# Kernel tuning notes

Measured on AMD Instinct MI355X. Metric: run time of the kernel, lower is better.

## Reference

```python
import jax, jax.numpy as jnp
import numpy as np

H, W = 2048, 2048
S = 10            # depth_segments
BOTTOM_PCT = 1    # bottom_percent
P_MIX = 0.5       # p
F_SCALE = 2.0     # f


def setup_inputs() -> dict:
    key = jax.random.key(0)
    k1, k2 = jax.random.split(key)
    image = jax.random.uniform(k1, (3, H, W), dtype=jnp.float32)
    # the |d_nbr - d_ctr| < 1 threshold gives a non-trivial bilateral mask.
    depth = jax.random.uniform(k2, (H, W), dtype=jnp.float32) * 5.0
    mu0 = jnp.ones((), dtype=jnp.float32)
    mu1 = jnp.ones((), dtype=jnp.float32)
    mu2 = jnp.ones((), dtype=jnp.float32)
    return {"image": image, "depth": depth, "mu0": mu0, "mu1": mu1, "mu2": mu2}


def _eigm_forward(image, depth, mu0, mu1, mu2):
    Hh, Ww = depth.shape
    HW = Hh * Ww
    dt = image.dtype

    # --- ULAP depth prior: d = mu0 + mu1*max(g,b) + mu2*r ---
    r, g, b = image[0], image[1], image[2]
    d = mu0 + mu1 * jnp.maximum(g, b) + mu2 * r                    # [H,W]

    # --- per-depth-bin background light B_c and direct signal D_c ---
    bins = jnp.linspace(depth.min(), depth.max(), S + 1)           # [S+1]
    seg = (depth[None] >= bins[:-1, None, None]) & (depth[None] < bins[1:, None, None])  # [S,H,W] bool
    seg_flat = seg.reshape(S, HW)
    n = seg_flat.sum(axis=1)                                       # [S] pixels per bin

    min_rgb = image.min(axis=0).reshape(HW)                        # darkest channel per pixel
    vals = jnp.where(seg_flat, min_rgb[None, :], jnp.asarray(np.inf, dt))
    svals = jnp.sort(vals, axis=1)                                 # segment pixels first, inf padding last
    k = (n * BOTTOM_PCT) // 100                                    # topk(largest=False) count per bin
    take = jnp.arange(HW)[None, :] < k[:, None]
    B_c = jnp.sum(jnp.where(take, svals, jnp.asarray(0.0, dt)), axis=1) / k.astype(dt)  # [S]

    segf = seg.astype(dt)
    seg_mean = jnp.einsum('chw,shw->sc', image, segf) / n.astype(dt)[:, None]  # [S,3]
    D_seg = seg_mean - B_c[:, None]                                # [S,3] per-segment direct signal
    # scatter each segment's D_c to its pixels -> per-pixel map [1,3,H,W]
    D = jnp.einsum('shw,sc->chw', segf, D_seg)[None]

    # --- depth-thresholded 3x3 local average (bilateral-style stencil) ---
    dpad = jnp.pad(depth, 1, constant_values=np.inf)               # inf => out-of-bounds invalid
    Dpad = jnp.pad(D, ((0, 0), (0, 0), (1, 1), (1, 1)))
    num = jnp.zeros_like(D)
    cnt = jnp.zeros((1, 1, Hh, Ww), dt)
    one = jnp.asarray(1.0, dt)
    for dy in (-1, 0, 1):
        for dx in (-1, 0, 1):
            nd = dpad[1 + dy:1 + dy + Hh, 1 + dx:1 + dx + Ww]
            valid = (jnp.abs(nd - depth) < one).astype(dt)[None, None]
            nD = Dpad[:, :, 1 + dy:1 + dy + Hh, 1 + dx:1 + dx + Ww]
            num = num + valid * nD
            cnt = cnt + valid
    a_prime = num / cnt                                            # center always valid -> cnt >= 1
    a_c = P_MIX * D + (1.0 - P_MIX) * a_prime

    E_c = F_SCALE * a_c                                            # [1,3,H,W]
    J_c = E_c * d[None, None]                                      # restored direct signal
    return J_c


def reference(image, depth, mu0, mu1, mu2):
    return _eigm_forward(image, depth, mu0, mu1, mu2)
```

## Files before the change

### kernel.cpp

```cpp
#include <hip/hip_runtime.h>
#include <cstdint>
#include <math.h>

#define HH 2048
#define WW 2048
#define HWPX (HH*WW)
#define NSEG 10
#define NB 128
#define HIST_WORDS (NSEG*NB)
#define NSHARD 8
#define LOWR 0.03125f
#define INV_LOWW 4096.0f
#define BINW (LOWR/(float)NB)

#define K1_BLOCKS 512
#define K2_BLOCKS 2048
#define NTH1 (K1_BLOCKS*256)
#define NTH2 (K2_BLOCKS*256)

typedef float vfloat4 __attribute__((ext_vector_type(4)));

#define WS_BMM 0
#define WS_HIST 1024
#define WS_ACC 11264
#define WS_DSEG 93184
#define WS_DMM (WS_DSEG + 44)
#define WS_DVAL (WS_DSEG + 48)

__device__ __forceinline__ int seg_of(float v, float dmin, float dmax, float invw) {
    int sg = (int)((v - dmin) * invw);
    sg = sg > (NSEG-1) ? (NSEG-1) : sg;
    return (v >= dmax) ? NSEG : sg;
}

__global__ __launch_bounds__(256) void k1_minmax(const float* __restrict__ depth,
                                                 uint32_t* __restrict__ wsu) {
    float* wsf = (float*)wsu;
    if (blockIdx.x == 0) {
        for (int j = threadIdx.x; j < NSHARD*HIST_WORDS; j += 256) wsu[WS_HIST + j] = 0u;
    }
    int tid = blockIdx.x * 256 + threadIdx.x;
    float vmin = INFINITY, vmax = 0.0f;
    const float4* d4 = (const float4*)depth;
    #pragma unroll
    for (int m = 0; m < HWPX/4/NTH1; ++m) {
        float4 v = d4[tid + m*NTH1];
        vmin = fminf(vmin, fminf(fminf(v.x, v.y), fminf(v.z, v.w)));
        vmax = fmaxf(vmax, fmaxf(fmaxf(v.x, v.y), fmaxf(v.z, v.w)));
    }
    #pragma unroll
    for (int off = 32; off > 0; off >>= 1) {
        vmin = fminf(vmin, __shfl_down(vmin, off, 64));
        vmax = fmaxf(vmax, __shfl_down(vmax, off, 64));
    }
    __shared__ float smin[4], smax[4];
    int wid = threadIdx.x >> 6;
    if ((threadIdx.x & 63) == 0) { smin[wid] = vmin; smax[wid] = vmax; }
    __syncthreads();
    if (threadIdx.x == 0) {
        wsf[WS_BMM + blockIdx.x]             = fminf(fminf(smin[0], smin[1]), fminf(smin[2], smin[3]));
        wsf[WS_BMM + K1_BLOCKS + blockIdx.x] = fmaxf(fmaxf(smax[0], smax[1]), fmaxf(smax[2], smax[3]));
    }
}

__device__ __forceinline__ void block_minmax(const float* wsf, float& dmin, float& dmax,
                                             float smn[4], float smx[4]) {
    float v0 = fminf(wsf[WS_BMM + threadIdx.x], wsf[WS_BMM + 256 + threadIdx.x]);
    float v1 = fmaxf(wsf[WS_BMM + K1_BLOCKS + threadIdx.x],
                     wsf[WS_BMM + K1_BLOCKS + 256 + threadIdx.x]);
    #pragma unroll
    for (int off = 32; off > 0; off >>= 1) {
        v0 = fminf(v0, __shfl_down(v0, off, 64));
        v1 = fmaxf(v1, __shfl_down(v1, off, 64));
    }
    int wid = threadIdx.x >> 6;
    if ((threadIdx.x & 63) == 0) { smn[wid] = v0; smx[wid] = v1; }
    __syncthreads();
    dmin = fminf(fminf(smn[0], smn[1]), fminf(smn[2], smn[3]));
    dmax = fmaxf(fmaxf(smx[0], smx[1]), fmaxf(smx[2], smx[3]));
}

__global__ __launch_bounds__(256, 4) void k2_hist(const float* __restrict__ image,
                                                  const float* __restrict__ depth,
                                                  const float* __restrict__ mu0p,
                                                  const float* __restrict__ mu1p,
                                                  const float* __restrict__ mu2p,
                                                  uint32_t* __restrict__ wsu) {
    __shared__ uint32_t s_hist[HIST_WORDS];
    __shared__ float s_red[4][40];
    __shared__ float smn[4], smx[4];
    float* wsf = (float*)wsu;
    for (int j = threadIdx.x; j < HIST_WORDS; j += 256) s_hist[j] = 0;

    float dmin, dmax;
    block_minmax(wsf, dmin, dmax, smn, smx);
    float invw = 10.0f / (dmax - dmin);
    float mu0 = *mu0p, mu1 = *mu1p, mu2 = *mu2p;

    float c_cnt[NSEG], c_r[NSEG], c_g[NSEG], c_b[NSEG];
    #pragma unroll
    for (int s = 0; s < NSEG; ++s) { c_cnt[s]=0.f; c_r[s]=0.f; c_g[s]=0.f; c_b[s]=0.f; }

    const float4* r4 = (const float4*)image;
    const float4* g4 = (const float4*)(image + HWPX);
    const float4* b4 = (const float4*)(image + 2*HWPX);
    const float4* d4 = (const float4*)depth;
    vfloat4* dval4 = (vfloat4*)(wsf + WS_DVAL);
    int tid = blockIdx.x * 256 + threadIdx.x;

    #pragma unroll
    for (int m = 0; m < HWPX/4/NTH2; ++m) {
        int i = tid + m*NTH2;
        float4 rv = r4[i], gv = g4[i], bv = b4[i], dv = d4[i];
        float ra[4] = {rv.x, rv.y, rv.z, rv.w};
        float ga[4] = {gv.x, gv.y, gv.z, gv.w};
        float ba[4] = {bv.x, bv.y, bv.z, bv.w};
        float da[4] = {dv.x, dv.y, dv.z, dv.w};
        float dvo[4];
        #pragma unroll
        for (int j = 0; j < 4; ++j) {
            int sg = seg_of(da[j], dmin, dmax, invw);
            float m2 = fminf(ra[j], fminf(ga[j], ba[j]));
            if (sg < NSEG && m2 < LOWR) {
                atomicAdd(&s_hist[sg*NB + (int)(m2 * INV_LOWW)], 1u);
            }
            #pragma unroll
            for (int s = 0; s < NSEG; ++s) {
                float sel = (sg == s) ? 1.0f : 0.0f;
                c_cnt[s] += sel;
                c_r[s] += sel * ra[j];
                c_g[s] += sel * ga[j];
                c_b[s] += sel * ba[j];
            }
            dvo[j] = mu0 + mu1 * fmaxf(ga[j], ba[j]) + mu2 * ra[j];
        }
        vfloat4 dq = {dvo[0], dvo[1], dvo[2], dvo[3]};
        dval4[i] = dq;
    }
    #pragma unroll
    for (int s = 0; s < NSEG; ++s) {
        #pragma unroll
        for (int off = 32; off > 0; off >>= 1) {
            c_cnt[s] += __shfl_down(c_cnt[s], off, 64);
            c_r[s]   += __shfl_down(c_r[s],   off, 64);
            c_g[s]   += __shfl_down(c_g[s],   off, 64);
            c_b[s]   += __shfl_down(c_b[s],   off, 64);
        }
    }
    int wid = threadIdx.x >> 6;
    if ((threadIdx.x & 63) == 0) {
        #pragma unroll
        for (int s = 0; s < NSEG; ++s) {
            s_red[wid][s]      = c_cnt[s];
            s_red[wid][10 + s] = c_r[s];
            s_red[wid][20 + s] = c_g[s];
            s_red[wid][30 + s] = c_b[s];
        }
    }
    __syncthreads();
    uint32_t* shard = wsu + WS_HIST + (blockIdx.x & (NSHARD-1)) * HIST_WORDS;
    for (int j = threadIdx.x; j < HIST_WORDS; j += 256) {
        uint32_t v = s_hist[j];
        if (v) atomicAdd(&shard[j], v);
    }
    if (threadIdx.x < 40) {
        float v = s_red[0][threadIdx.x] + s_red[1][threadIdx.x]
                + s_red[2][threadIdx.x] + s_red[3][threadIdx.x];
        wsf[WS_ACC + blockIdx.x*40 + threadIdx.x] = v;
    }
}

__global__ void k3_stats(uint32_t* __restrict__ wsu) {
    __shared__ uint32_t s_hist[HIST_WORDS];
    __shared__ float s_part[16][40];
    __shared__ float s_acc[40];
    __shared__ float smn[4], smx[4];
    float* wsf = (float*)wsu;
    for (int j = threadIdx.x; j < HIST_WORDS; j += 256) {
        uint32_t acc = 0;
        #pragma unroll
        for (int c = 0; c < NSHARD; ++c) acc += wsu[WS_HIST + c*HIST_WORDS + j];
        s_hist[j] = acc;
    }
    for (int q = threadIdx.x; q < 16*40; q += 256) {
        int y = q / 40, j = q - y*40;
        const float* p = wsf + WS_ACC + (size_t)(y*(K2_BLOCKS/16))*40 + j;
        float acc = 0.0f;
        #pragma unroll 8
        for (int b = 0; b < K2_BLOCKS/16; ++b) acc += p[b*40];
        s_part[y][j] = acc;
    }
    float dmin, dmax;
    block_minmax(wsf, dmin, dmax, smn, smx);
    if (threadIdx.x < 40) {
        float t = 0.0f;
        #pragma unroll
        for (int y = 0; y < 16; ++y) t += s_part[y][threadIdx.x];
        s_acc[threadIdx.x] = t;
    }
    __syncthreads();
    int s = threadIdx.x;
    if (s < NSEG) {
        float fn = s_acc[s];
        uint32_t n = (uint32_t)(fn + 0.5f);
        uint32_t k = n / 100;
        const uint32_t* h = &s_hist[s*NB];
        float bsum = 0.0f; uint32_t taken = 0;
        for (int b = 0; b < NB; ++b) {
            uint32_t rem = k - taken;
            uint32_t c = h[b];
            uint32_t t = c < rem ? c : rem;
            bsum += (float)t * (((float)b + 0.5f) * BINW);
            taken += t;
        }
        if (taken < k) bsum += (float)(k - taken) * LOWR;
        float B = (k > 0) ? (bsum / (float)k) : 0.0f;
        wsf[WS_DSEG + s*4 + 0] = s_acc[10 + s] / fn - B;
        wsf[WS_DSEG + s*4 + 1] = s_acc[20 + s] / fn - B;
        wsf[WS_DSEG + s*4 + 2] = s_acc[30 + s] / fn - B;
        wsf[WS_DSEG + s*4 + 3] = 0.0f;
    } else if (s == NSEG) {
        wsf[WS_DSEG + 40] = 0.0f; wsf[WS_DSEG + 41] = 0.0f;
        wsf[WS_DSEG + 42] = 0.0f; wsf[WS_DSEG + 43] = 0.0f;
    } else if (s == NSEG+1) {
        wsf[WS_DMM] = dmin; wsf[WS_DMM + 1] = dmax;
    }
}

__global__ __launch_bounds__(256, 2) void k4_out(const float* __restrict__ depth,
                                                 const uint32_t* __restrict__ wsu,
                                                 float* __restrict__ out) {
    __shared__ float4 s_D4[NSEG+1];
    const float* wsf = (const float*)wsu;
    if (threadIdx.x < NSEG+1)
        s_D4[threadIdx.x] = ((const float4*)(wsf + WS_DSEG))[threadIdx.x];
    __syncthreads();

    float dmin = wsf[WS_DMM];
    float dmax = wsf[WS_DMM + 1];
    float invw = 10.0f / (dmax - dmin);

    int gid = blockIdx.x * 256 + threadIdx.x;
    int row = gid >> 9;
    int col = (gid & 511) << 2;
    int lane = threadIdx.x & 63;

    float4 dva4 = ((const float4*)(wsf + WS_DVAL))[gid];

    float nd[3][6];
    #pragma unroll
    for (int rr = 0; rr < 3; ++rr) {
        int r2 = row + rr - 1;
        if (r2 >= 0 && r2 < HH) {
            const float* dp = depth + (size_t)r2 * WW + col;
            float4 m = *(const float4*)dp;
            float left  = __shfl_up(m.w, 1, 64);
            float right = __shfl_down(m.x, 1, 64);
            if (lane == 0)  left  = (col > 0)      ? dp[-1] : INFINITY;
            if (lane == 63) right = (col + 4 < WW) ? dp[4]  : INFINITY;
            nd[rr][0] = left;  nd[rr][1] = m.x; nd[rr][2] = m.y;
            nd[rr][3] = m.z;   nd[rr][4] = m.w; nd[rr][5] = right;
        } else {
            #pragma unroll
            for (int cc = 0; cc < 6; ++cc) nd[rr][cc] = INFINITY;
        }
    }

    float cnt[4], A0[4], A1[4], A2[4];
    #pragma unroll
    for (int j = 0; j < 4; ++j) { cnt[j]=0.f; A0[j]=0.f; A1[j]=0.f; A2[j]=0.f; }

    #pragma unroll
    for (int rr = 0; rr < 3; ++rr) {
        #pragma unroll
        for (int cc = 0; cc < 6; ++cc) {
            float nv = nd[rr][cc];
            float4 dd = s_D4[seg_of(nv, dmin, dmax, invw)];
            #pragma unroll
            for (int j = 0; j < 4; ++j) {
                if (j >= cc - 2 && j <= cc) {
                    float msk = (fabsf(nv - nd[1][j+1]) < 1.0f) ? 1.0f : 0.0f;
                    cnt[j] += msk; A0[j] += msk*dd.x; A1[j] += msk*dd.y; A2[j] += msk*dd.z;
                }
            }
        }
    }

    float dva[4] = {dva4.x, dva4.y, dva4.z, dva4.w};
    float o0[4], o1[4], o2[4];
    #pragma unroll
    for (int j = 0; j < 4; ++j) {
        float rc = 1.0f / cnt[j];
        float4 Dc = s_D4[seg_of(nd[1][j+1], dmin, dmax, invw)];
        o0[j] = (Dc.x + A0[j]*rc) * dva[j];
        o1[j] = (Dc.y + A1[j]*rc) * dva[j];
        o2[j] = (Dc.z + A2[j]*rc) * dva[j];
    }
    size_t base = (size_t)row * WW + col;
    vfloat4 v0 = {o0[0], o0[1], o0[2], o0[3]};
    vfloat4 v1 = {o1[0], o1[1], o1[2], o1[3]};
    vfloat4 v2 = {o2[0], o2[1], o2[2], o2[3]};
    __builtin_nontemporal_store(v0, (vfloat4*)(out + base));
    __builtin_nontemporal_store(v1, (vfloat4*)(out + HWPX + base));
    __builtin_nontemporal_store(v2, (vfloat4*)(out + 2*HWPX + base));
}

extern "C" void kernel_launch(void* const* d_in, const int* in_sizes, int n_in,
                              void* d_out, int out_size, void* d_ws, size_t ws_size,
                              hipStream_t stream) {
    const float* image = (const float*)d_in[0];
    const float* depth = (const float*)d_in[1];
    const float* mu0   = (const float*)d_in[2];
    const float* mu1   = (const float*)d_in[3];
    const float* mu2   = (const float*)d_in[4];
    uint32_t* wsu = (uint32_t*)d_ws;
    float* out = (float*)d_out;

    hipLaunchKernelGGL(k1_minmax, dim3(K1_BLOCKS), dim3(256), 0, stream, depth, wsu);
    hipLaunchKernelGGL(k2_hist,   dim3(K2_BLOCKS), dim3(256), 0, stream,
                       image, depth, mu0, mu1, mu2, wsu);
    hipLaunchKernelGGL(k3_stats,  dim3(1),         dim3(256), 0, stream, wsu);
    hipLaunchKernelGGL(k4_out,    dim3((HWPX/4)/256), dim3(256), 0, stream,
                       depth, wsu, out);
}
```

Baseline: 173.6 us.

## Fuse stats reduction into histogram kernel via last-block-done atomic counter

Removes the separate single-block stats kernel launch by having the last k2 block, found through an agent-scope atomic counter, do the final reduction of histogram shards and per-block sums. It also cuts the k2 grid from 2048 to 512 blocks with a grid-stride loop and relaxes launch bounds to 2 blocks per CU, so there are fewer partial sums to reduce and more registers per thread. In exchange, the tail reduction still runs serially inside one block, and fewer blocks may hide memory latency less well.

```diff
diff --git a/kernel.cpp b/kernel.cpp
--- a/kernel.cpp
+++ b/kernel.cpp
@@ -14,18 +14,18 @@
 #define BINW (LOWR/(float)NB)
 
 #define K1_BLOCKS 512
-#define K2_BLOCKS 2048
-#define NTH1 (K1_BLOCKS*256)
-#define NTH2 (K2_BLOCKS*256)
+#define K2_BLOCKS 512
+#define NTH (K2_BLOCKS*256)
 
 typedef float vfloat4 __attribute__((ext_vector_type(4)));
 
 #define WS_BMM 0
 #define WS_HIST 1024
-#define WS_ACC 11264
-#define WS_DSEG 93184
+#define WS_CNT 11264
+#define WS_ACC 11280
+#define WS_DSEG 31760
 #define WS_DMM (WS_DSEG + 44)
-#define WS_DVAL (WS_DSEG + 48)
+#define WS_DVAL 31808
 
 __device__ __forceinline__ int seg_of(float v, float dmin, float dmax, float invw) {
     int sg = (int)((v - dmin) * invw);
@@ -38,13 +38,13 @@
     float* wsf = (float*)wsu;
     if (blockIdx.x == 0) {
         for (int j = threadIdx.x; j < NSHARD*HIST_WORDS; j += 256) wsu[WS_HIST + j] = 0u;
+        if (threadIdx.x == 0) wsu[WS_CNT] = 0u;
     }
     int tid = blockIdx.x * 256 + threadIdx.x;
     float vmin = INFINITY, vmax = 0.0f;
     const float4* d4 = (const float4*)depth;
-    #pragma unroll
-    for (int m = 0; m < HWPX/4/NTH1; ++m) {
-        float4 v = d4[tid + m*NTH1];
+    for (int i = tid; i < HWPX/4; i += NTH) {
+        float4 v = d4[i];
         vmin = fminf(vmin, fminf(fminf(v.x, v.y), fminf(v.z, v.w)));
         vmax = fmaxf(vmax, fmaxf(fmaxf(v.x, v.y), fmaxf(v.z, v.w)));
     }
@@ -80,7 +80,7 @@
     dmax = fmaxf(fmaxf(smx[0], smx[1]), fmaxf(smx[2], smx[3]));
 }
 
-__global__ __launch_bounds__(256, 4) void k2_hist(const float* __restrict__ image,
+__global__ __launch_bounds__(256, 2) void k2_hist(const float* __restrict__ image,
                                                   const float* __restrict__ depth,
                                                   const float* __restrict__ mu0p,
                                                   const float* __restrict__ mu1p,
@@ -88,7 +88,10 @@
                                                   uint32_t* __restrict__ wsu) {
     __shared__ uint32_t s_hist[HIST_WORDS];
     __shared__ float s_red[4][40];
+    __shared__ float s_part[16][40];
+    __shared__ float s_acc[40];
     __shared__ float smn[4], smx[4];
+    __shared__ int s_last;
     float* wsf = (float*)wsu;
     for (int j = threadIdx.x; j < HIST_WORDS; j += 256) s_hist[j] = 0;
 
@@ -107,10 +110,7 @@
     const float4* d4 = (const float4*)depth;
     vfloat4* dval4 = (vfloat4*)(wsf + WS_DVAL);
     int tid = blockIdx.x * 256 + threadIdx.x;
-
-    #pragma unroll
-    for (int m = 0; m < HWPX/4/NTH2; ++m) {
-        int i = tid + m*NTH2;
+    for (int i = tid; i < HWPX/4; i += NTH) {
         float4 rv = r4[i], gv = g4[i], bv = b4[i], dv = d4[i];
         float ra[4] = {rv.x, rv.y, rv.z, rv.w};
         float ga[4] = {gv.x, gv.y, gv.z, gv.w};
@@ -168,30 +168,38 @@
                 + s_red[2][threadIdx.x] + s_red[3][threadIdx.x];
         wsf[WS_ACC + blockIdx.x*40 + threadIdx.x] = v;
     }
-}
-
-__global__ void k3_stats(uint32_t* __restrict__ wsu) {
-    __shared__ uint32_t s_hist[HIST_WORDS];
-    __shared__ float s_part[16][40];
-    __shared__ float s_acc[40];
-    __shared__ float smn[4], smx[4];
-    float* wsf = (float*)wsu;
+
+    __threadfence();
+    if (threadIdx.x == 0) {
+        uint32_t old = __hip_atomic_fetch_add(&wsu[WS_CNT], 1u,
+                                              __ATOMIC_ACQ_REL, __HIP_MEMORY_SCOPE_AGENT);
+        s_last = (old == K2_BLOCKS - 1) ? 1 : 0;
+    }
+    __syncthreads();
+    if (!s_last) return;
+    __threadfence();
+
     for (int j = threadIdx.x; j < HIST_WORDS; j += 256) {
         uint32_t acc = 0;
         #pragma unroll
-        for (int c = 0; c < NSHARD; ++c) acc += wsu[WS_HIST + c*HIST_WORDS + j];
+        for (int c = 0; c < NSHARD; ++c)
+            acc += __hip_atomic_load(&wsu[WS_HIST + c*HIST_WORDS + j],
+                                     __ATOMIC_RELAXED, __HIP_MEMORY_SCOPE_AGENT);
         s_hist[j] = acc;
     }
     for (int q = threadIdx.x; q < 16*40; q += 256) {
         int y = q / 40, j = q - y*40;
-        const float* p = wsf + WS_ACC + (size_t)(y*(K2_BLOCKS/16))*40 + j;
+        const uint32_t* p = wsu + WS_ACC + (size_t)(y*32)*40 + j;
         float acc = 0.0f;
-        #pragma unroll 8
-        for (int b = 0; b < K2_BLOCKS/16; ++b) acc += p[b*40];
+        #pragma unroll
+        for (int b = 0; b < 32; ++b) {
+            uint32_t u = __hip_atomic_load(&p[(size_t)b*40],
+                                           __ATOMIC_RELAXED, __HIP_MEMORY_SCOPE_AGENT);
+            acc += __uint_as_float(u);
+        }
         s_part[y][j] = acc;
     }
-    float dmin, dmax;
-    block_minmax(wsf, dmin, dmax, smn, smx);
+    __syncthreads();
     if (threadIdx.x < 40) {
         float t = 0.0f;
         #pragma unroll
@@ -319,7 +327,6 @@
     hipLaunchKernelGGL(k1_minmax, dim3(K1_BLOCKS), dim3(256), 0, stream, depth, wsu);
     hipLaunchKernelGGL(k2_hist,   dim3(K2_BLOCKS), dim3(256), 0, stream,
                        image, depth, mu0, mu1, mu2, wsu);
-    hipLaunchKernelGGL(k3_stats,  dim3(1),         dim3(256), 0, stream, wsu);
     hipLaunchKernelGGL(k4_out,    dim3((HWPX/4)/256), dim3(256), 0, stream,
                        depth, wsu, out);
 }
```

Measured after the change: 181.2 us. 4.4% more time.
